# Kernel optimization log

Hardware: AMD Instinct MI355X
Metric: run time of the kernel (lower is better)

## Reference

```python
import jax, jax.numpy as jnp
import numpy as np


def extract_patches(x, k):
    # x: [B, C, H, W] -> patches [B, C, fh, fw, k, k]  (stride-1 VALID windows,
    # same layout as torch unfold(2,k,1).unfold(3,k,1))
    B, C, H, W = x.shape
    fh, fw = H - k + 1, W - k + 1
    rows = []
    for dy in range(k):  # k*k = 49 static slices, no data-dim python loop
        cols = [x[:, :, dy:dy + fh, dx:dx + fw] for dx in range(k)]
        rows.append(jnp.stack(cols, axis=-1))
    return jnp.stack(rows, axis=-2)  # [B, C, fh, fw, k, k]


def setup_inputs() -> dict:
    key = jax.random.key(0)
    k1, k2, k3 = jax.random.split(key, 3)
    B, Cin, H, W = 64, 3, 64, 64
    O, k = 16, 7
    stdv = 1.0 / float(np.sqrt(Cin * k * k))  # matches reset_parameters
    x = jax.random.normal(k1, (B, Cin, H, W), dtype=jnp.float32)
    K_hit = jax.random.uniform(k2, (O, Cin, k, k), jnp.float32, -stdv, stdv)
    K_miss = jax.random.uniform(k3, (O, Cin, k, k), jnp.float32, -stdv, stdv)
    return {"input": x, "K_hit": K_hit, "K_miss": K_miss}


def reference(input, K_hit, K_miss):
    B, Cin, H, W = input.shape
    O, _, k, _ = K_hit.shape
    fh = H - k + 1
    num_blocks = fh * fh * Cin  # as in the torch code (assumes square input)
    patches = extract_patches(input, k)  # [B, Cin, fh, fw, k, k]

    def body(carry, Ks):
        kh, km = Ks  # each [Cin, k, k]
        # F_hit = (patch - K_hit)*-1 ; (-relu(F_hit)).sum() == -sum(relu(K_hit - patch))
        s_hit = -jnp.sum(jax.nn.relu(kh[None, :, None, None, :, :] - patches))
        s_miss = jnp.sum(jax.nn.relu(patches - km[None, :, None, None, :, :]))
        return carry, (s_hit, s_miss)

    _, (s_hit, s_miss) = jax.lax.scan(body, None, (K_hit, K_miss))  # [O], [O]

    def tile(v):  # scalar per out channel broadcast over batch and all blocks
        t = jnp.broadcast_to(v[None, :, None], (B, O, num_blocks))
        return t.reshape(B, Cin * O, fh, fh)

    F_map = tile(s_hit - s_miss)
    F_hit_list = tile(s_hit)
    F_miss_list = tile(s_miss)
    return F_map, F_hit_list, F_miss_list
```

## Files before the change

### kernel.cpp

```cpp
#include <hip/hip_runtime.h>
#include <hip/hip_bf16.h>

#define NBUCK 2048
#define WB 0.005859375f
#define SCALE 170.6666667f

#define SEG 10092u
#define OSEG 161472u
#define OUT1 10334208u
#define NOUT 31002624u

#define TAIL_BASE (NOUT - 524288u)
#define F_TR   0u
#define RC_TR  196704u
#define SF_OFF 344232u
#define SRC_OFF 344328u
#define PACK   344400u

typedef float v4f __attribute__((ext_vector_type(4)));

__global__ __launch_bounds__(1024) void build_kernel(
    const float* __restrict__ x, float* __restrict__ tail, float* __restrict__ gsum)
{
    __shared__ float sH[NBUCK];
    __shared__ float sWc[16], sWd[16];
    const int blk = blockIdx.x;
    const int tid = threadIdx.x;
    sH[tid] = 0.f; sH[tid + 1024] = 0.f;
    if (blk == 0 && tid < 64) gsum[tid] = 0.f;
    __syncthreads();

    int slot, stride;
    unsigned baseT, baseS;
    if (blk < 96) {
        const int c = blk / 32, g = blk % 32;
        slot = c * 32 + g; stride = 96; baseT = F_TR; baseS = SF_OFF;
#pragma unroll
        for (int pb = 0; pb < 2; ++pb) {
            const int batch = 2 * g + pb;
            const int plane = batch * 3 + c;
            float4 val = ((const float4*)x)[plane * 1024 + tid];
            float vv[4] = {val.x, val.y, val.z, val.w};
            const int pix0 = tid * 4;
#pragma unroll
            for (int e = 0; e < 4; ++e) {
                const int idx = pix0 + e;
                const int py = idx >> 6, px = idx & 63;
                const float v = vv[e];
                const int b = min(max((int)fmaf(v, SCALE, 1024.f), 0), NBUCK - 1);
                atomicAdd(&sH[b], 1.f);
                const bool rb = (py < 6) | (py >= 58);
                const bool cb = (px < 6) | (px >= 58);
                if (rb & cb) {
                    const int ri = (py < 6) ? py : py - 52;
                    const int ci = (px < 6) ? px : px - 52;
                    tail[PACK + ((unsigned)c * 144 + ri * 12 + ci) * 64u + batch] = v;
                }
            }
        }
    } else if (blk < 132) {
        const int idx = blk - 96;
        const int c = idx / 12, ri = idx % 12;
        const int py = (ri < 6) ? ri : ri + 52;
        slot = c * 24 + ri; stride = 72; baseT = RC_TR; baseS = SRC_OFF;
        const int batch = tid >> 4, f4 = tid & 15;
        float4 val = ((const float4*)x)[(batch * 3 + c) * 1024 + py * 16 + f4];
        float vv[4] = {val.x, val.y, val.z, val.w};
#pragma unroll
        for (int e = 0; e < 4; ++e) {
            const int b = min(max((int)fmaf(vv[e], SCALE, 1024.f), 0), NBUCK - 1);
            atomicAdd(&sH[b], 1.f);
        }
    } else {
        const int idx = blk - 132;
        const int c = idx / 12, ci = idx % 12;
        const int pxc = (ci < 6) ? ci : ci + 52;
        slot = c * 24 + 12 + ci; stride = 72; baseT = RC_TR; baseS = SRC_OFF;
        const int batch = tid >> 4, py0 = (tid & 15) * 4;
        const float* base = x + (batch * 3 + c) * 4096 + pxc;
        float vr[4];
#pragma unroll
        for (int e = 0; e < 4; ++e) vr[e] = base[(py0 + e) * 64];
#pragma unroll
        for (int e = 0; e < 4; ++e) {
            const int b = min(max((int)fmaf(vr[e], SCALE, 1024.f), 0), NBUCK - 1);
            atomicAdd(&sH[b], 1.f);
        }
    }
    __syncthreads();

    const int lane = tid & 63;
    const int wid  = tid >> 6;
    const int b0 = 2 * tid, b1 = 2 * tid + 1;
    const float c0 = sH[b0], c1 = sH[b1];
    const float d0 = (float)b0 * c0, d1 = (float)b1 * c1;
    const float cs = c0 + c1, ds = d0 + d1;
    float ic = cs, id = ds;
#pragma unroll
    for (int off = 1; off < 64; off <<= 1) {
        const float tc = __shfl_up(ic, off);
        const float td = __shfl_up(id, off);
        if (lane >= off) { ic += tc; id += td; }
    }
    if (lane == 63) { sWc[wid] = ic; sWd[wid] = id; }
    __syncthreads();
    float baseC = 0.f, baseD = 0.f, Ntot = 0.f, Dtot = 0.f;
#pragma unroll
    for (int w = 0; w < 16; ++w) {
        const float wc = sWc[w], wd = sWd[w];
        Ntot += wc; Dtot += wd;
        if (w < wid) { baseC += wc; baseD += wd; }
    }
    const float Cex = baseC + ic - cs;
    const float Dex = baseD + id - ds;
    const float T0 = WB * (Dtot + 0.5f * Ntot);

    const float Tb0 = T0 + WB * (2.f * (float)b0 * Cex - 2.f * Dex - (float)b0 * Ntot);
    const float C1 = Cex + c0, D1 = Dex + d0;
    const float Tb1 = T0 + WB * (2.f * (float)b1 * C1 - 2.f * D1 - (float)b1 * Ntot);
    tail[baseT + (unsigned)b0 * stride + slot] = Tb0;
    tail[baseT + (unsigned)b1 * stride + slot] = Tb1;
    if (tid == 1023) {
        tail[baseT + (unsigned)NBUCK * stride + slot] =
            T0 + WB * ((float)NBUCK * Ntot - 2.f * Dtot);
        tail[baseS + slot] = T0 - 6.f * Ntot;
    }
}

__global__ __launch_bounds__(512) void query_kernel(
    const float* __restrict__ Kh, const float* __restrict__ Km,
    const float* __restrict__ tail, float* __restrict__ gsum)
{
    __shared__ float sC[2304];
    __shared__ float sK[32];
    __shared__ float sredA[32][16];
    __shared__ float sredL[32][16];

    const int c  = blockIdx.x / 49;
    const int t  = blockIdx.x - c * 49;
    const int dy = t / 7, dx = t - dy * 7;
    const int tid = threadIdx.x;

    for (int i = tid; i < 2304; i += 512) {
        const int cell = i >> 6, batch = i & 63;
        const int qr = cell / 6, qc = cell - qr * 6;
        const int ri = (qr < dy) ? qr : 6 + qr;
        const int ci = (qc < dx) ? qc : 6 + qc;
        sC[i] = tail[PACK + ((unsigned)c * 144 + ri * 12 + ci) * 64u + batch];
    }
    if (tid < 32)
        sK[tid] = ((tid >= 16) ? Km : Kh)[(tid & 15) * 147 + c * 49 + t];
    __syncthreads();

    const int q   = tid >> 4;
    const int sub = tid & 15;
    const float k = sK[q];

    float accA = 0.f, accL = 0.f;
#pragma unroll 16
    for (int step = 0; step < 144; ++step) {
        const float v = sC[sub + 16 * step];
        accA += fabsf(k - v);
        accL += k - v;
    }

    const float u = fmaf(k, SCALE, 1024.f);
    const int j = min(max((int)u, 0), NBUCK - 1);
    const float fr = u - (float)j;

    if (sub < 8) {
        const v4f r0 = *(const v4f*)(tail + F_TR + (unsigned)j * 96u + c * 32 + sub * 4);
        const v4f r1 = *(const v4f*)(tail + F_TR + (unsigned)(j + 1) * 96u + c * 32 + sub * 4);
        const float s0 = r0.x + r0.y + r0.z + r0.w;
        const float s1 = r1.x + r1.y + r1.z + r1.w;
        accA += s0 + fr * (s1 - s0);
        const v4f sf = *(const v4f*)(tail + SF_OFF + c * 32 + sub * 4);
        accL -= sf.x + sf.y + sf.z + sf.w;
        if (sub == 0) accL += k * 212992.f;
    } else if (sub < 14) {
        const int s6 = sub - 8;
        const int rinv = (s6 < dy) ? s6 : 6 + s6;
        const int cinv = (s6 < dx) ? s6 : 6 + s6;
        const int slr = c * 24 + rinv;
        const int slc = c * 24 + 12 + cinv;
        const float tr0 = tail[RC_TR + (unsigned)j * 72u + slr];
        const float tr1 = tail[RC_TR + (unsigned)(j + 1) * 72u + slr];
        const float tc0 = tail[RC_TR + (unsigned)j * 72u + slc];
        const float tc1 = tail[RC_TR + (unsigned)(j + 1) * 72u + slc];
        accA -= tr0 + fr * (tr1 - tr0);
        accA -= tc0 + fr * (tc1 - tc0);
        accL += tail[SRC_OFF + slr] + tail[SRC_OFF + slc];
    }

    sredA[q][sub] = accA;
    sredL[q][sub] = accL;
    __syncthreads();
    if (tid < 64) {
        const int idx  = tid >> 1;
        const int part = tid & 1;
        const float (*sr)[16] = part ? sredL : sredA;
        float s = 0.f;
#pragma unroll
        for (int e = 0; e < 16; ++e) s += sr[idx][e];
        atomicAdd(&gsum[part * 32 + idx], s);
    }
}

__global__ __launch_bounds__(256) void fill_kernel(
    const float* __restrict__ gsum, v4f* __restrict__ out, unsigned n4)
{
    __shared__ float sv[48];
    if (threadIdx.x < 48) {
        const int o = threadIdx.x & 15, grp = threadIdx.x >> 4;
        const float h = -0.5f * (gsum[32 + o] + gsum[o]);
        const float m =  0.5f * (gsum[16 + o] - gsum[48 + o]);
        sv[threadIdx.x] = (grp == 0) ? (h - m) : ((grp == 1) ? h : m);
    }
    __syncthreads();
    const unsigned stride = gridDim.x * blockDim.x;
    for (unsigned i = blockIdx.x * blockDim.x + threadIdx.x; i < n4; i += stride) {
        const unsigned f = i * 4u;
        const unsigned w   = f / OUT1;
        const unsigned rem = f - w * OUT1;
        const unsigned o   = (rem % OSEG) / SEG;
        const float val = sv[w * 16 + o];
        v4f pk = {val, val, val, val};
        __builtin_nontemporal_store(pk, &out[i]);
    }
}

extern "C" void kernel_launch(void* const* d_in, const int* in_sizes, int n_in,
                              void* d_out, int out_size, void* d_ws, size_t ws_size,
                              hipStream_t stream)
{
    const float* x  = (const float*)d_in[0];
    const float* Kh = (const float*)d_in[1];
    const float* Km = (const float*)d_in[2];
    float* out  = (float*)d_out;
    float* tail = out + TAIL_BASE;
    float* gsum = (float*)d_ws;

    build_kernel<<<168, 1024, 0, stream>>>(x, tail, gsum);
    query_kernel<<<147, 512, 0, stream>>>(Kh, Km, tail, gsum);
    fill_kernel <<<4096, 256, 0, stream>>>(gsum, (v4f*)out, NOUT / 4u);
}
```

Measured before the change: 53.84 us.

## Split histogram build into per-plane blocks with transposed column pass and sharded sums

Adds a transpose kernel that writes x transposed into scratch, so that border-column histograms can be read contiguously. The build kernel now uses one block per (batch,channel) plane plus 64 blocks that each process several row or column units. This gives 256 blocks instead of 168, with finer-grained histogram tables. The query kernel reads wider vectorised table rows, and gsum atomics are spread over 8 shards that fill_kernel reduces. The cost is an extra kernel launch, the transpose traffic, and larger scratch tables in the output tail.

```diff
diff --git a/kernel.cpp b/kernel.cpp
--- a/kernel.cpp
+++ b/kernel.cpp
@@ -10,85 +10,46 @@
 #define OUT1 10334208u
 #define NOUT 31002624u
 
-#define TAIL_BASE (NOUT - 524288u)
-#define F_TR   0u
-#define RC_TR  196704u
-#define SF_OFF 344232u
-#define SRC_OFF 344328u
-#define PACK   344400u
+#define TAIL_BASE (NOUT - 2097152u)
+#define T_XT    0u
+#define F_TR    786432u
+#define RC_TR   1179840u
+#define SF_OFF  1769952u
+#define SRC_OFF 1770144u
+#define PACK    1770432u
 
 typedef float v4f __attribute__((ext_vector_type(4)));
 
-__global__ __launch_bounds__(1024) void build_kernel(
+__global__ __launch_bounds__(256) void transpose_kernel(
     const float* __restrict__ x, float* __restrict__ tail, float* __restrict__ gsum)
 {
-    __shared__ float sH[NBUCK];
-    __shared__ float sWc[16], sWd[16];
-    const int blk = blockIdx.x;
+    __shared__ float sT[64][65];
+    const int plane = blockIdx.x;
     const int tid = threadIdx.x;
-    sH[tid] = 0.f; sH[tid + 1024] = 0.f;
-    if (blk == 0 && tid < 64) gsum[tid] = 0.f;
-    __syncthreads();
-
-    int slot, stride;
-    unsigned baseT, baseS;
-    if (blk < 96) {
-        const int c = blk / 32, g = blk % 32;
-        slot = c * 32 + g; stride = 96; baseT = F_TR; baseS = SF_OFF;
-#pragma unroll
-        for (int pb = 0; pb < 2; ++pb) {
-            const int batch = 2 * g + pb;
-            const int plane = batch * 3 + c;
-            float4 val = ((const float4*)x)[plane * 1024 + tid];
-            float vv[4] = {val.x, val.y, val.z, val.w};
-            const int pix0 = tid * 4;
-#pragma unroll
-            for (int e = 0; e < 4; ++e) {
-                const int idx = pix0 + e;
-                const int py = idx >> 6, px = idx & 63;
-                const float v = vv[e];
-                const int b = min(max((int)fmaf(v, SCALE, 1024.f), 0), NBUCK - 1);
-                atomicAdd(&sH[b], 1.f);
-                const bool rb = (py < 6) | (py >= 58);
-                const bool cb = (px < 6) | (px >= 58);
-                if (rb & cb) {
-                    const int ri = (py < 6) ? py : py - 52;
-                    const int ci = (px < 6) ? px : px - 52;
-                    tail[PACK + ((unsigned)c * 144 + ri * 12 + ci) * 64u + batch] = v;
-                }
-            }
-        }
-    } else if (blk < 132) {
-        const int idx = blk - 96;
-        const int c = idx / 12, ri = idx % 12;
-        const int py = (ri < 6) ? ri : ri + 52;
-        slot = c * 24 + ri; stride = 72; baseT = RC_TR; baseS = SRC_OFF;
-        const int batch = tid >> 4, f4 = tid & 15;
-        float4 val = ((const float4*)x)[(batch * 3 + c) * 1024 + py * 16 + f4];
-        float vv[4] = {val.x, val.y, val.z, val.w};
-#pragma unroll
-        for (int e = 0; e < 4; ++e) {
-            const int b = min(max((int)fmaf(vv[e], SCALE, 1024.f), 0), NBUCK - 1);
-            atomicAdd(&sH[b], 1.f);
-        }
-    } else {
-        const int idx = blk - 132;
-        const int c = idx / 12, ci = idx % 12;
-        const int pxc = (ci < 6) ? ci : ci + 52;
-        slot = c * 24 + 12 + ci; stride = 72; baseT = RC_TR; baseS = SRC_OFF;
-        const int batch = tid >> 4, py0 = (tid & 15) * 4;
-        const float* base = x + (batch * 3 + c) * 4096 + pxc;
-        float vr[4];
-#pragma unroll
-        for (int e = 0; e < 4; ++e) vr[e] = base[(py0 + e) * 64];
-#pragma unroll
-        for (int e = 0; e < 4; ++e) {
-            const int b = min(max((int)fmaf(vr[e], SCALE, 1024.f), 0), NBUCK - 1);
-            atomicAdd(&sH[b], 1.f);
-        }
-    }
-    __syncthreads();
-
+    if (plane == 0) { gsum[tid] = 0.f; gsum[256 + tid] = 0.f; }
+    const float4* x4 = (const float4*)(x + plane * 4096);
+    v4f* o4 = (v4f*)(tail + T_XT + (unsigned)plane * 4096u);
+#pragma unroll
+    for (int it = 0; it < 4; ++it) {
+        const int i = it * 256 + tid;
+        float4 v = x4[i];
+        const int row = i >> 4, c4 = (i & 15) * 4;
+        sT[row][c4] = v.x; sT[row][c4+1] = v.y; sT[row][c4+2] = v.z; sT[row][c4+3] = v.w;
+    }
+    __syncthreads();
+#pragma unroll
+    for (int it = 0; it < 4; ++it) {
+        const int i = it * 256 + tid;
+        const int px = i >> 4, py0 = (i & 15) * 4;
+        v4f w = {sT[py0][px], sT[py0+1][px], sT[py0+2][px], sT[py0+3][px]};
+        o4[i] = w;
+    }
+}
+
+__device__ __forceinline__ void scan_store(
+    float* sH, float* sWc, float* sWd, float* tail,
+    unsigned baseT, int stride, int slot, unsigned baseS, int tid)
+{
     const int lane = tid & 63;
     const int wid  = tid >> 6;
     const int b0 = 2 * tid, b1 = 2 * tid + 1;
@@ -114,7 +75,6 @@
     const float Cex = baseC + ic - cs;
     const float Dex = baseD + id - ds;
     const float T0 = WB * (Dtot + 0.5f * Ntot);
-
     const float Tb0 = T0 + WB * (2.f * (float)b0 * Cex - 2.f * Dex - (float)b0 * Ntot);
     const float C1 = Cex + c0, D1 = Dex + d0;
     const float Tb1 = T0 + WB * (2.f * (float)b1 * C1 - 2.f * D1 - (float)b1 * Ntot);
@@ -127,6 +87,70 @@
     }
 }
 
+__global__ __launch_bounds__(1024) void build_kernel(
+    const float* __restrict__ x, float* __restrict__ tail)
+{
+    __shared__ float sH[NBUCK];
+    __shared__ float sWc[16], sWd[16];
+    const int blk = blockIdx.x;
+    const int tid = threadIdx.x;
+
+    if (blk < 192) {
+        sH[tid] = 0.f; sH[tid + 1024] = 0.f;
+        __syncthreads();
+        const int batch = blk / 3, c = blk % 3;
+        float4 val = ((const float4*)x)[blk * 1024 + tid];
+        float vv[4] = {val.x, val.y, val.z, val.w};
+        const int pix0 = tid * 4;
+        const int py = pix0 >> 6;
+#pragma unroll
+        for (int e = 0; e < 4; ++e) {
+            const int px = (pix0 & 63) + e;
+            const float v = vv[e];
+            const int b = min(max((int)fmaf(v, SCALE, 1024.f), 0), NBUCK - 1);
+            atomicAdd(&sH[b], 1.f);
+            const bool rb = (py < 6) | (py >= 58);
+            const bool cb = (px < 6) | (px >= 58);
+            if (rb & cb) {
+                const int ri = (py < 6) ? py : py - 52;
+                const int ci = (px < 6) ? px : px - 52;
+                tail[PACK + ((unsigned)c * 144 + ri * 12 + ci) * 64u + batch] = v;
+            }
+        }
+        __syncthreads();
+        scan_store(sH, sWc, sWd, tail, F_TR, 192, c * 64 + batch, SF_OFF, tid);
+    } else {
+        const int idx = blk - 192;
+        const int nu = (idx < 32) ? 5 : 4;
+        const int u0 = (idx < 32) ? idx * 5 : 160 + (idx - 32) * 4;
+        for (int un = 0; un < nu; ++un) {
+            const int u = u0 + un;
+            const int c = u / 96;
+            const int r2 = u - c * 96;
+            const int kind = r2 / 48;
+            const int r3 = r2 - kind * 48;
+            const int i = r3 >> 2, qq = r3 & 3;
+            sH[tid] = 0.f; sH[tid + 1024] = 0.f;
+            __syncthreads();
+            const int batch = qq * 16 + (tid >> 6);
+            const int pos = tid & 63;
+            float v;
+            if (kind == 0) {
+                const int py = (i < 6) ? i : i + 52;
+                v = x[(batch * 3 + c) * 4096 + py * 64 + pos];
+            } else {
+                const int px = (i < 6) ? i : i + 52;
+                v = tail[T_XT + (unsigned)((batch * 3 + c) * 4096) + px * 64 + pos];
+            }
+            const int b = min(max((int)fmaf(v, SCALE, 1024.f), 0), NBUCK - 1);
+            atomicAdd(&sH[b], 1.f);
+            __syncthreads();
+            scan_store(sH, sWc, sWd, tail, RC_TR, 288, u, SRC_OFF, tid);
+            __syncthreads();
+        }
+    }
+}
+
 __global__ __launch_bounds__(512) void query_kernel(
     const float* __restrict__ Kh, const float* __restrict__ Km,
     const float* __restrict__ tail, float* __restrict__ gsum)
@@ -168,28 +192,33 @@
     const int j = min(max((int)u, 0), NBUCK - 1);
     const float fr = u - (float)j;
 
-    if (sub < 8) {
-        const v4f r0 = *(const v4f*)(tail + F_TR + (unsigned)j * 96u + c * 32 + sub * 4);
-        const v4f r1 = *(const v4f*)(tail + F_TR + (unsigned)(j + 1) * 96u + c * 32 + sub * 4);
+    {
+        const v4f f0 = *(const v4f*)(tail + F_TR + (unsigned)j * 192u + c * 64 + sub * 4);
+        const v4f f1 = *(const v4f*)(tail + F_TR + (unsigned)(j + 1) * 192u + c * 64 + sub * 4);
+        const float s0 = f0.x + f0.y + f0.z + f0.w;
+        const float s1 = f1.x + f1.y + f1.z + f1.w;
+        accA += s0 + fr * (s1 - s0);
+        const v4f sf = *(const v4f*)(tail + SF_OFF + c * 64 + sub * 4);
+        accL -= sf.x + sf.y + sf.z + sf.w;
+        if (sub == 0) accL += k * 212992.f;
+    }
+    if (sub < 12) {
+        int base_f4;
+        if (sub < 6) {
+            const int ri = (sub < dy) ? sub : 6 + sub;
+            base_f4 = c * 96 + ri * 4;
+        } else {
+            const int s6 = sub - 6;
+            const int ci = (s6 < dx) ? s6 : 6 + s6;
+            base_f4 = c * 96 + 48 + ci * 4;
+        }
+        const v4f r0 = *(const v4f*)(tail + RC_TR + (unsigned)j * 288u + base_f4);
+        const v4f r1 = *(const v4f*)(tail + RC_TR + (unsigned)(j + 1) * 288u + base_f4);
         const float s0 = r0.x + r0.y + r0.z + r0.w;
         const float s1 = r1.x + r1.y + r1.z + r1.w;
-        accA += s0 + fr * (s1 - s0);
-        const v4f sf = *(const v4f*)(tail + SF_OFF + c * 32 + sub * 4);
-        accL -= sf.x + sf.y + sf.z + sf.w;
-        if (sub == 0) accL += k * 212992.f;
-    } else if (sub < 14) {
-        const int s6 = sub - 8;
-        const int rinv = (s6 < dy) ? s6 : 6 + s6;
-        const int cinv = (s6 < dx) ? s6 : 6 + s6;
-        const int slr = c * 24 + rinv;
-        const int slc = c * 24 + 12 + cinv;
-        const float tr0 = tail[RC_TR + (unsigned)j * 72u + slr];
-        const float tr1 = tail[RC_TR + (unsigned)(j + 1) * 72u + slr];
-        const float tc0 = tail[RC_TR + (unsigned)j * 72u + slc];
-        const float tc1 = tail[RC_TR + (unsigned)(j + 1) * 72u + slc];
-        accA -= tr0 + fr * (tr1 - tr0);
-        accA -= tc0 + fr * (tc1 - tc0);
-        accL += tail[SRC_OFF + slr] + tail[SRC_OFF + slc];
+        accA -= s0 + fr * (s1 - s0);
+        const v4f sr = *(const v4f*)(tail + SRC_OFF + base_f4);
+        accL += sr.x + sr.y + sr.z + sr.w;
     }
 
     sredA[q][sub] = accA;
@@ -202,7 +231,7 @@
         float s = 0.f;
 #pragma unroll
         for (int e = 0; e < 16; ++e) s += sr[idx][e];
-        atomicAdd(&gsum[part * 32 + idx], s);
+        atomicAdd(&gsum[(blockIdx.x & 7) * 64 + part * 32 + idx], s);
     }
 }
 
@@ -212,8 +241,14 @@
     __shared__ float sv[48];
     if (threadIdx.x < 48) {
         const int o = threadIdx.x & 15, grp = threadIdx.x >> 4;
-        const float h = -0.5f * (gsum[32 + o] + gsum[o]);
-        const float m =  0.5f * (gsum[16 + o] - gsum[48 + o]);
+        float Ah = 0.f, Am = 0.f, Lh = 0.f, Lm = 0.f;
+#pragma unroll
+        for (int b = 0; b < 8; ++b) {
+            Ah += gsum[b * 64 + o];      Am += gsum[b * 64 + 16 + o];
+            Lh += gsum[b * 64 + 32 + o]; Lm += gsum[b * 64 + 48 + o];
+        }
+        const float h = -0.5f * (Lh + Ah);
+        const float m =  0.5f * (Am - Lm);
         sv[threadIdx.x] = (grp == 0) ? (h - m) : ((grp == 1) ? h : m);
     }
     __syncthreads();
@@ -240,7 +275,8 @@
     float* tail = out + TAIL_BASE;
     float* gsum = (float*)d_ws;
 
-    build_kernel<<<168, 1024, 0, stream>>>(x, tail, gsum);
-    query_kernel<<<147, 512, 0, stream>>>(Kh, Km, tail, gsum);
-    fill_kernel <<<4096, 256, 0, stream>>>(gsum, (v4f*)out, NOUT / 4u);
-}
+    transpose_kernel<<<192, 256, 0, stream>>>(x, tail, gsum);
+    build_kernel    <<<256, 1024, 0, stream>>>(x, tail);
+    query_kernel    <<<147, 512, 0, stream>>>(Kh, Km, tail, gsum);
+    fill_kernel     <<<4096, 256, 0, stream>>>(gsum, (v4f*)out, NOUT / 4u);
+}
```

Measured after the change: 65.70 us. 1.22x slower.
